# Optimization experiments

Hardware: AMD Instinct MI355X
Metric: run time of the kernel (lower is better)

Reference implementation:

```python
import jax, jax.numpy as jnp
import numpy as np

NUM_NEURONS = 4_000_000
NUM_WEIGHTS = 8
SRC_SIZE = 2_000_000


def setup_inputs() -> dict:
    key = jax.random.key(0)
    k1, k2, k3, k4, k5, k6 = jax.random.split(key, 6)
    values_a = jax.random.normal(k1, (SRC_SIZE,), dtype=jnp.float32)
    values_b = jax.random.normal(k2, (SRC_SIZE,), dtype=jnp.float32)
    weights = jax.random.normal(k3, (NUM_WEIGHTS,), dtype=jnp.float32)
    idx_a = jax.random.randint(k4, (SRC_SIZE,), 0, SRC_SIZE, dtype=jnp.int64 if jax.config.jax_enable_x64 else jnp.int32).astype(jnp.int32)
    idx_b = jax.random.randint(k5, (SRC_SIZE,), 0, SRC_SIZE).astype(jnp.int32)
    concat_idx = jax.random.randint(k6, (NUM_NEURONS * NUM_WEIGHTS,), 0, 2 * SRC_SIZE).astype(jnp.int32)
    return {
        "values_a": values_a,
        "values_b": values_b,
        "weights": weights,
        "idx_a": idx_a,
        "idx_b": idx_b,
        "concat_idx": concat_idx,
    }


def reference(values_a, values_b, weights, idx_a, idx_b, concat_idx):
    # GatherModule stage 1: per-source-layer gather of needed ordinals, concatenated
    # in layer order.  [2*SRC_SIZE]
    layer_inputs_needed = jnp.concatenate([values_a[idx_a], values_b[idx_b]])
    # GatherModule stage 2: one entry per (neuron, input) pair.  [NUM_NEURONS*NUM_WEIGHTS]
    gathered = layer_inputs_needed[concat_idx]
    # WeightedRuleLayer: per-input-position weights shared across all neurons,
    # weighted sum over rule-body inputs + tanh activation.  [NUM_NEURONS]
    g = gathered.reshape(-1, weights.shape[0])
    return jnp.tanh(jnp.einsum("nk,k->n", g, weights))
```

## Files before the change

### kernel.cpp

```cpp
#include <hip/hip_runtime.h>
#include <hip/hip_fp16.h>

constexpr int SRC = 2000000;
constexpr int NN  = 4000000;

typedef int v4i __attribute__((ext_vector_type(4)));

__global__ __launch_bounds__(256) void build_table_f16(
    const float* __restrict__ va, const float* __restrict__ vb,
    const int*   __restrict__ ia, const int*   __restrict__ ib,
    __half* __restrict__ table)
{
    const int total4 = (2 * SRC) / 4;
    const int half4  = SRC / 4;
    const int stride = gridDim.x * blockDim.x;
    for (int i = blockIdx.x * blockDim.x + threadIdx.x; i < total4; i += stride) {
        float4 r;
        if (i < half4) {
            int4 idx = reinterpret_cast<const int4*>(ia)[i];
            r.x = va[idx.x]; r.y = va[idx.y]; r.z = va[idx.z]; r.w = va[idx.w];
        } else {
            int4 idx = reinterpret_cast<const int4*>(ib)[i - half4];
            r.x = vb[idx.x]; r.y = vb[idx.y]; r.z = vb[idx.z]; r.w = vb[idx.w];
        }
        unsigned int h0 = __half_as_ushort(__float2half_rn(r.x));
        unsigned int h1 = __half_as_ushort(__float2half_rn(r.y));
        unsigned int h2 = __half_as_ushort(__float2half_rn(r.z));
        unsigned int h3 = __half_as_ushort(__float2half_rn(r.w));
        uint2 p;
        p.x = h0 | (h1 << 16);
        p.y = h2 | (h3 << 16);
        reinterpret_cast<uint2*>(table)[i] = p;
    }
}

__global__ __launch_bounds__(256) void neuron_f16(
    const int*   __restrict__ cidx,
    const __half* __restrict__ table,
    const float* __restrict__ w,
    float* __restrict__ out)
{
    __shared__ float ws[8];
    if (threadIdx.x < 8) ws[threadIdx.x] = w[threadIdx.x];
    __syncthreads();
    const float w0 = ws[0], w1 = ws[1], w2 = ws[2], w3 = ws[3];
    const float w4 = ws[4], w5 = ws[5], w6 = ws[6], w7 = ws[7];

    const int stride = gridDim.x * blockDim.x;
    for (int n = blockIdx.x * blockDim.x + threadIdx.x; n < NN; n += stride) {
        const v4i* p = reinterpret_cast<const v4i*>(cidx) + (size_t)n * 2;
        v4i c0 = __builtin_nontemporal_load(p);
        v4i c1 = __builtin_nontemporal_load(p + 1);
        float acc = __half2float(table[c0.x]) * w0
                  + __half2float(table[c0.y]) * w1
                  + __half2float(table[c0.z]) * w2
                  + __half2float(table[c0.w]) * w3
                  + __half2float(table[c1.x]) * w4
                  + __half2float(table[c1.y]) * w5
                  + __half2float(table[c1.z]) * w6
                  + __half2float(table[c1.w]) * w7;
        __builtin_nontemporal_store(tanhf(acc), &out[n]);
    }
}

__global__ __launch_bounds__(256) void fused_kernel(
    const float* __restrict__ va, const float* __restrict__ vb,
    const int*   __restrict__ ia, const int*   __restrict__ ib,
    const int*   __restrict__ cidx,
    const float* __restrict__ w,
    float* __restrict__ out)
{
    __shared__ float ws[8];
    if (threadIdx.x < 8) ws[threadIdx.x] = w[threadIdx.x];
    __syncthreads();

    const int stride = gridDim.x * blockDim.x;
    for (int n = blockIdx.x * blockDim.x + threadIdx.x; n < NN; n += stride) {
        const int4* p = reinterpret_cast<const int4*>(cidx) + (size_t)n * 2;
        int4 c0 = p[0];
        int4 c1 = p[1];
        int c[8] = {c0.x, c0.y, c0.z, c0.w, c1.x, c1.y, c1.z, c1.w};
        float acc = 0.f;
        #pragma unroll
        for (int k = 0; k < 8; ++k) {
            int ci = c[k];
            float v = (ci < SRC) ? va[ia[ci]] : vb[ib[ci - SRC]];
            acc += v * ws[k];
        }
        out[n] = tanhf(acc);
    }
}

extern "C" void kernel_launch(void* const* d_in, const int* in_sizes, int n_in,
                              void* d_out, int out_size, void* d_ws, size_t ws_size,
                              hipStream_t stream) {
    const float* va   = (const float*)d_in[0];
    const float* vb   = (const float*)d_in[1];
    const float* w    = (const float*)d_in[2];
    const int*   ia   = (const int*)d_in[3];
    const int*   ib   = (const int*)d_in[4];
    const int*   cidx = (const int*)d_in[5];
    float* out = (float*)d_out;

    const size_t table_bytes = (size_t)(2 * SRC) * sizeof(__half);
    if (ws_size >= table_bytes) {
        __half* table = (__half*)d_ws;
        build_table_f16<<<2048, 256, 0, stream>>>(va, vb, ia, ib, table);
        neuron_f16<<<2048, 256, 0, stream>>>(cidx, table, w, out);
    } else {
        fused_kernel<<<2048, 256, 0, stream>>>(va, vb, ia, ib, cidx, w, out);
    }
}
```

Measured before the change: 501.6 us.

## Split table build and neuron gather into range-partitioned passes for cache locality

Table construction now runs as four passes, each gathering only source indices from one half of the value array, so each pass touches an 8MB-or-smaller working set. The neuron stage is split into two passes over the cidx array: the first accumulates terms whose table index falls in the lower half and stores a partial sum, and the second adds the upper-half terms and applies tanh. The goal is to keep the randomly gathered region small enough to stay cache-resident. The cost is reading the 128MB cidx array twice, plus extra reads and writes of the index arrays and the partial-sum output.

```diff
diff --git a/kernel.cpp b/kernel.cpp
--- a/kernel.cpp
+++ b/kernel.cpp
@@ -3,42 +3,30 @@
 
 constexpr int SRC = 2000000;
 constexpr int NN  = 4000000;
+constexpr int TBL = 2 * SRC;
+constexpr int HALF_TBL = TBL / 2;
 
 typedef int v4i __attribute__((ext_vector_type(4)));
 
-__global__ __launch_bounds__(256) void build_table_f16(
-    const float* __restrict__ va, const float* __restrict__ vb,
-    const int*   __restrict__ ia, const int*   __restrict__ ib,
-    __half* __restrict__ table)
+__global__ __launch_bounds__(256) void build_chunk(
+    const float* __restrict__ v, const int* __restrict__ idx,
+    __half* __restrict__ tout, int lo, int hi)
 {
-    const int total4 = (2 * SRC) / 4;
-    const int half4  = SRC / 4;
     const int stride = gridDim.x * blockDim.x;
-    for (int i = blockIdx.x * blockDim.x + threadIdx.x; i < total4; i += stride) {
-        float4 r;
-        if (i < half4) {
-            int4 idx = reinterpret_cast<const int4*>(ia)[i];
-            r.x = va[idx.x]; r.y = va[idx.y]; r.z = va[idx.z]; r.w = va[idx.w];
-        } else {
-            int4 idx = reinterpret_cast<const int4*>(ib)[i - half4];
-            r.x = vb[idx.x]; r.y = vb[idx.y]; r.z = vb[idx.z]; r.w = vb[idx.w];
+    for (int i = blockIdx.x * blockDim.x + threadIdx.x; i < SRC; i += stride) {
+        int c = __builtin_nontemporal_load(&idx[i]);
+        if (c >= lo && c < hi) {
+            tout[i] = __float2half_rn(v[c]);
         }
-        unsigned int h0 = __half_as_ushort(__float2half_rn(r.x));
-        unsigned int h1 = __half_as_ushort(__float2half_rn(r.y));
-        unsigned int h2 = __half_as_ushort(__float2half_rn(r.z));
-        unsigned int h3 = __half_as_ushort(__float2half_rn(r.w));
-        uint2 p;
-        p.x = h0 | (h1 << 16);
-        p.y = h2 | (h3 << 16);
-        reinterpret_cast<uint2*>(table)[i] = p;
     }
 }
 
-__global__ __launch_bounds__(256) void neuron_f16(
-    const int*   __restrict__ cidx,
+template<int PHASE>
+__global__ __launch_bounds__(256) void neuron_pass(
+    const int*    __restrict__ cidx,
     const __half* __restrict__ table,
-    const float* __restrict__ w,
-    float* __restrict__ out)
+    const float*  __restrict__ w,
+    float*        __restrict__ po)
 {
     __shared__ float ws[8];
     if (threadIdx.x < 8) ws[threadIdx.x] = w[threadIdx.x];
@@ -51,15 +39,20 @@
         const v4i* p = reinterpret_cast<const v4i*>(cidx) + (size_t)n * 2;
         v4i c0 = __builtin_nontemporal_load(p);
         v4i c1 = __builtin_nontemporal_load(p + 1);
-        float acc = __half2float(table[c0.x]) * w0
-                  + __half2float(table[c0.y]) * w1
-                  + __half2float(table[c0.z]) * w2
-                  + __half2float(table[c0.w]) * w3
-                  + __half2float(table[c1.x]) * w4
-                  + __half2float(table[c1.y]) * w5
-                  + __half2float(table[c1.z]) * w6
-                  + __half2float(table[c1.w]) * w7;
-        __builtin_nontemporal_store(tanhf(acc), &out[n]);
+
+        float acc;
+        if (PHASE == 0) acc = 0.0f;
+        else            acc = __builtin_nontemporal_load(&po[n]);
+
+        #define TERM(c, wk)                                                  \
+            if (PHASE == 0 ? ((c) < HALF_TBL) : ((c) >= HALF_TBL))           \
+                acc += __half2float(table[(c)]) * (wk);
+        TERM(c0.x, w0) TERM(c0.y, w1) TERM(c0.z, w2) TERM(c0.w, w3)
+        TERM(c1.x, w4) TERM(c1.y, w5) TERM(c1.z, w6) TERM(c1.w, w7)
+        #undef TERM
+
+        if (PHASE == 0) __builtin_nontemporal_store(acc, &po[n]);
+        else            __builtin_nontemporal_store(tanhf(acc), &po[n]);
     }
 }
 
@@ -102,11 +95,16 @@
     const int*   cidx = (const int*)d_in[5];
     float* out = (float*)d_out;
 
-    const size_t table_bytes = (size_t)(2 * SRC) * sizeof(__half);
+    const size_t table_bytes = (size_t)TBL * sizeof(__half);
     if (ws_size >= table_bytes) {
         __half* table = (__half*)d_ws;
-        build_table_f16<<<2048, 256, 0, stream>>>(va, vb, ia, ib, table);
-        neuron_f16<<<2048, 256, 0, stream>>>(cidx, table, w, out);
+        const int HS = SRC / 2;
+        build_chunk<<<2048, 256, 0, stream>>>(va, ia, table,        0,  HS);
+        build_chunk<<<2048, 256, 0, stream>>>(va, ia, table,       HS, SRC);
+        build_chunk<<<2048, 256, 0, stream>>>(vb, ib, table + SRC,  0,  HS);
+        build_chunk<<<2048, 256, 0, stream>>>(vb, ib, table + SRC, HS, SRC);
+        neuron_pass<0><<<2048, 256, 0, stream>>>(cidx, table, w, out);
+        neuron_pass<1><<<2048, 256, 0, stream>>>(cidx, table, w, out);
     } else {
         fused_kernel<<<2048, 256, 0, stream>>>(va, vb, ia, ib, cidx, w, out);
     }
```

Result: faster. 427.5 us (-14.8%).
